# Performance work log

Hardware: AMD Instinct MI355X
Metric: run time of the kernel (lower is better)

The kernel has to match this reference:

```python
import jax, jax.numpy as jnp
import numpy as np

M, N, K, C, G = 16384, 131072, 16, 128, 8
EPS_BN = 1e-5


def _bn(x, g, b):
    # inference-mode BatchNorm1d (running_mean=0, running_var=1)
    return x * (g / jnp.sqrt(1.0 + EPS_BN)) + b


def setup_inputs() -> dict:
    key = jax.random.key(0)
    ks = jax.random.split(key, 16)
    f32 = jnp.float32
    s = 0.05
    return {
        "query_feat": jax.random.normal(ks[0], (M, C), f32),
        "context_feat": jax.random.normal(ks[1], (N, C), f32),
        "query_coord": jax.random.normal(ks[2], (M, 3), f32),
        "context_coord": jax.random.normal(ks[3], (N, 3), f32),
        "Wq": jax.random.normal(ks[4], (C, C), f32) * s,
        "bq": jnp.zeros((C,), f32),
        "gq": jnp.ones((C,), f32),
        "betaq": jnp.zeros((C,), f32),
        "Wk": jax.random.normal(ks[5], (C, C), f32) * s,
        "bk": jnp.zeros((C,), f32),
        "gk": jnp.ones((C,), f32),
        "betak": jnp.zeros((C,), f32),
        "Wv": jax.random.normal(ks[6], (C, C), f32) * s,
        "bv": jnp.zeros((C,), f32),
        "Wp1": jax.random.normal(ks[7], (3, C), f32) * s,
        "bp1": jnp.zeros((C,), f32),
        "gp1": jnp.ones((C,), f32),
        "betap1": jnp.zeros((C,), f32),
        "Wp2": jax.random.normal(ks[8], (C, C), f32) * s,
        "bp2": jnp.zeros((C,), f32),
        "Ww1": jax.random.normal(ks[9], (C, G), f32) * s,
        "bw1": jnp.zeros((G,), f32),
        "gw1": jnp.ones((G,), f32),
        "betaw1": jnp.zeros((G,), f32),
        "Ww2": jax.random.normal(ks[10], (G, G), f32) * s,
        "bw2": jnp.zeros((G,), f32),
        "knn_indexes": jax.random.randint(ks[11], (M, K), 0, N, dtype=jnp.int32),
    }


def reference(query_feat, context_feat, query_coord, context_coord,
              Wq, bq, gq, betaq, Wk, bk, gk, betak, Wv, bv,
              Wp1, bp1, gp1, betap1, Wp2, bp2,
              Ww1, bw1, gw1, betaw1, Ww2, bw2, knn_indexes):
    q = jax.nn.relu(_bn(query_feat @ Wq + bq, gq, betaq))              # (M, C)
    k = jax.nn.relu(_bn(context_feat @ Wk + bk, gk, betak))            # (N, C)
    v = context_feat @ Wv + bv                                         # (N, C)

    mask = knn_indexes >= 0                                            # (M, K); -1 = padded neighbor
    idx = jnp.where(mask, knn_indexes, 0)
    mf = mask[..., None].astype(q.dtype)                               # (M, K, 1)

    key_g = k[idx] * mf                                                # (M, K, C) gather (zero row for -1)
    val_g = v[idx] * mf                                                # (M, K, C)
    pos = (context_coord[idx] - query_coord[:, None, :]) * mf          # (M, K, 3) relative position

    # positional-encoding bias branch (pe_bias=True, pe_multiplier=False)
    peb = jax.nn.relu(_bn(pos @ Wp1 + bp1, gp1, betap1)) @ Wp2 + bp2   # (M, K, C)
    rel = key_g - q[:, None, :] + peb                                  # (M, K, C)
    val_g = val_g + peb

    # grouped vector attention weights
    w = jax.nn.relu(_bn(rel @ Ww1 + bw1, gw1, betaw1)) @ Ww2 + bw2     # (M, K, G)
    w = jax.nn.softmax(w, axis=1) * mf                                 # softmax over neighbors, mask padded

    m_, k_ = idx.shape
    c_ = q.shape[-1]
    g_ = w.shape[-1]
    out = jnp.einsum('mkgi,mkg->mgi', val_g.reshape(m_, k_, g_, c_ // g_), w)
    return out.reshape(m_, c_)
```

## Files before the change

### kernel.cpp

```cpp
#include <hip/hip_runtime.h>

#define C 128
#define G 8
#define KNN 16
#define QB 4
#define EPS 1e-5f

typedef unsigned short u16;
typedef __attribute__((ext_vector_type(8))) short short8;
typedef __attribute__((ext_vector_type(4))) float float4v;

union frag_u { short8 v; u16 u[8]; };

__device__ inline u16 f2bf(float f) {
    unsigned u = __builtin_bit_cast(unsigned, f);
    unsigned r = (u + 0x7fffu + ((u >> 16) & 1u)) >> 16;
    return (u16)r;
}
__device__ inline float bf2f(u16 h) {
    unsigned u = ((unsigned)h) << 16;
    return __builtin_bit_cast(float, u);
}

__global__ __launch_bounds__(256) void prep_w(
    const float* __restrict__ Wk, const float* __restrict__ Wv,
    const float* __restrict__ Wq, const float* __restrict__ Wp2,
    const float* __restrict__ Ww1, u16* __restrict__ dst)
{
    const int b = blockIdx.x, t = threadIdx.x;
    if (b < 4) {
        const float* W = b == 0 ? Wk : b == 1 ? Wv : b == 2 ? Wq : Wp2;
        u16* d = dst + b * 16384;
        for (int e = t; e < 16384; e += 256) {
            const int k = e >> 7, n = e & 127;
            const int cb = n >> 4, lan = n & 15;
            const int kk = k >> 5, quad = (k >> 3) & 3, j = k & 7;
            d[(((cb * 4 + kk) * 4 + quad) * 16 + lan) * 8 + j] = f2bf(W[e]);
        }
    } else {
        u16* d = dst + 4 * 16384;
        for (int e = t; e < 4096; e += 256) {
            const int j = e & 7, lan = (e >> 3) & 15;
            const int quad = (e >> 7) & 3, kk = e >> 9;
            const int k = kk * 32 + quad * 8 + j;
            d[e] = lan < 8 ? f2bf(Ww1[k * G + lan]) : (u16)0;
        }
    }
}

__global__ __launch_bounds__(256) void proj_kv(
    const float* __restrict__ X,
    const u16* __restrict__ PWk, const float* __restrict__ bk,
    const float* __restrict__ gk, const float* __restrict__ betak,
    const u16* __restrict__ PWv, const float* __restrict__ bv,
    u16* __restrict__ kout, u16* __restrict__ vout)
{
    __shared__ u16 Xs[64 * 136];
    __shared__ u16 Os[64 * 136];
    const int t = threadIdx.x;
    const int w = t >> 6, l = t & 63;
    const int quad = l >> 4, lan = l & 15;
    const long long row0 = (long long)blockIdx.x * 64;

    {
        const float4* Xv = (const float4*)(X + row0 * C);
#pragma unroll
        for (int i = 0; i < 8; i++) {
            const int e = t + 256 * i;
            const int r = e >> 5, c4 = e & 31;
            const float4 f = Xv[e];
            uint2 p;
            p.x = (unsigned)f2bf(f.x) | ((unsigned)f2bf(f.y) << 16);
            p.y = (unsigned)f2bf(f.z) | ((unsigned)f2bf(f.w) << 16);
            *(uint2*)(&Xs[r * 136 + c4 * 4]) = p;
        }
    }

    short8 Bf[2][2][4];
#pragma unroll
    for (int w2 = 0; w2 < 2; w2++) {
        const u16* P = w2 ? PWv : PWk;
#pragma unroll
        for (int ct = 0; ct < 2; ct++) {
            const int cb = w * 2 + ct;
#pragma unroll
            for (int kk = 0; kk < 4; kk++)
                Bf[w2][ct][kk] = *(const short8*)(P + (((cb * 4 + kk) * 4 + quad) * 16 + lan) * 8);
        }
    }
    __syncthreads();

    float4v acc[2][2][4];
#pragma unroll
    for (int w2 = 0; w2 < 2; w2++)
#pragma unroll
        for (int ct = 0; ct < 2; ct++)
#pragma unroll
            for (int rt = 0; rt < 4; rt++)
                acc[w2][ct][rt] = (float4v)0.f;

#pragma unroll
    for (int rt = 0; rt < 4; rt++) {
#pragma unroll
        for (int kk = 0; kk < 4; kk++) {
            const short8 A = *(const short8*)(&Xs[(rt * 16 + lan) * 136 + kk * 32 + quad * 8]);
#pragma unroll
            for (int w2 = 0; w2 < 2; w2++)
#pragma unroll
                for (int ct = 0; ct < 2; ct++)
                    acc[w2][ct][rt] = __builtin_amdgcn_mfma_f32_16x16x32_bf16(
                        A, Bf[w2][ct][kk], acc[w2][ct][rt], 0, 0, 0);
        }
    }

#pragma unroll
    for (int ct = 0; ct < 2; ct++) {
        const int cg = w * 32 + ct * 16 + lan;
        const float bb = bk[cg];
        const float sc = gk[cg] * rsqrtf(1.f + EPS);
        const float sh = betak[cg];
#pragma unroll
        for (int rt = 0; rt < 4; rt++)
#pragma unroll
            for (int reg = 0; reg < 4; reg++) {
                float y = (acc[0][ct][rt][reg] + bb) * sc + sh;
                y = y > 0.f ? y : 0.f;
                Os[(rt * 16 + quad * 4 + reg) * 136 + cg] = f2bf(y);
            }
    }
    __syncthreads();
#pragma unroll
    for (int i = 0; i < 4; i++) {
        const int e = t + 256 * i;
        const int r = e >> 4, cc = (e & 15) * 8;
        *(short8*)(kout + (row0 + r) * C + cc) = *(const short8*)(&Os[r * 136 + cc]);
    }
    __syncthreads();

#pragma unroll
    for (int ct = 0; ct < 2; ct++) {
        const int cg = w * 32 + ct * 16 + lan;
        const float bb = bv[cg];
#pragma unroll
        for (int rt = 0; rt < 4; rt++)
#pragma unroll
            for (int reg = 0; reg < 4; reg++)
                Os[(rt * 16 + quad * 4 + reg) * 136 + cg] = f2bf(acc[1][ct][rt][reg] + bb);
    }
    __syncthreads();
#pragma unroll
    for (int i = 0; i < 4; i++) {
        const int e = t + 256 * i;
        const int r = e >> 4, cc = (e & 15) * 8;
        *(short8*)(vout + (row0 + r) * C + cc) = *(const short8*)(&Os[r * 136 + cc]);
    }
}

__global__ __launch_bounds__(256) void attn4(
    const float* __restrict__ qfeat,
    const u16* __restrict__ kbuf, const u16* __restrict__ vbuf,
    const float* __restrict__ qcoord, const float* __restrict__ ccoord,
    const u16* __restrict__ PWq, const float* __restrict__ bq,
    const float* __restrict__ gq, const float* __restrict__ betaq,
    const float* __restrict__ Wp1, const float* __restrict__ bp1,
    const float* __restrict__ gp1, const float* __restrict__ betap1,
    const u16* __restrict__ PWp2, const float* __restrict__ bp2,
    const u16* __restrict__ PWw1, const float* __restrict__ bw1,
    const float* __restrict__ gw1, const float* __restrict__ betaw1,
    const float* __restrict__ Ww2, const float* __restrict__ bw2,
    const int* __restrict__ knn, float* __restrict__ out)
{
    __shared__ u16   fA[64 * 136];
    __shared__ u16   relB[64 * 136];
    __shared__ float qs[QB * C];
    __shared__ float pxs[64], pys[64], pzs[64], mfs[64];
    __shared__ float wl[QB * 16 * G];

    const int t = threadIdx.x;
    const int w = t >> 6, l = t & 63;
    const int quad = l >> 4, lan = l & 15;
    const int m0 = blockIdx.x * QB;

    const int rsub = t >> 4;
    const int c8 = (t & 15) * 8;
    float mfr[4];
    frag_u kg[4], vg[4];
#pragma unroll
    for (int p = 0; p < 4; p++) {
        const int ii = knn[m0 * KNN + p * 16 + rsub];
        mfr[p] = ii >= 0 ? 1.f : 0.f;
        const int i0 = ii >= 0 ? ii : 0;
        kg[p].v = *(const short8*)(kbuf + (size_t)i0 * C + c8);
        vg[p].v = *(const short8*)(vbuf + (size_t)i0 * C + c8);
    }

    {
        frag_u z;
        if (rsub < QB) {
            const float4 f0 = *(const float4*)(qfeat + (size_t)(m0 + rsub) * C + c8);
            const float4 f1 = *(const float4*)(qfeat + (size_t)(m0 + rsub) * C + c8 + 4);
            z.u[0] = f2bf(f0.x); z.u[1] = f2bf(f0.y);
            z.u[2] = f2bf(f0.z); z.u[3] = f2bf(f0.w);
            z.u[4] = f2bf(f1.x); z.u[5] = f2bf(f1.y);
            z.u[6] = f2bf(f1.z); z.u[7] = f2bf(f1.w);
        } else {
            z.v = (short8)0;
        }
        *(short8*)(&relB[rsub * 136 + c8]) = z.v;
    }
    if (t < 64) {
        const int q = t >> 4;
        const int ii = knn[m0 * KNN + t];
        const float mf = ii >= 0 ? 1.f : 0.f;
        const int i0 = ii >= 0 ? ii : 0;
        mfs[t] = mf;
        pxs[t] = (ccoord[i0 * 3 + 0] - qcoord[(m0 + q) * 3 + 0]) * mf;
        pys[t] = (ccoord[i0 * 3 + 1] - qcoord[(m0 + q) * 3 + 1]) * mf;
        pzs[t] = (ccoord[i0 * 3 + 2] - qcoord[(m0 + q) * 3 + 2]) * mf;
    }
    __syncthreads();

    {
        short8 Bq[2][4];
#pragma unroll
        for (int ct = 0; ct < 2; ct++) {
            const int cb = w * 2 + ct;
#pragma unroll
            for (int kk = 0; kk < 4; kk++)
                Bq[ct][kk] = *(const short8*)(PWq + (((cb * 4 + kk) * 4 + quad) * 16 + lan) * 8);
        }
        float4v aq[2];
        aq[0] = (float4v)0.f; aq[1] = (float4v)0.f;
#pragma unroll
        for (int kk = 0; kk < 4; kk++) {
            const short8 A = *(const short8*)(&relB[lan * 136 + kk * 32 + quad * 8]);
#pragma unroll
            for (int ct = 0; ct < 2; ct++)
                aq[ct] = __builtin_amdgcn_mfma_f32_16x16x32_bf16(A, Bq[ct][kk], aq[ct], 0, 0, 0);
        }
        if (quad == 0) {
#pragma unroll
            for (int ct = 0; ct < 2; ct++) {
                const int col = w * 32 + ct * 16 + lan;
                const float bb = bq[col];
                const float sc = gq[col] * rsqrtf(1.f + EPS);
                const float sh = betaq[col];
#pragma unroll
                for (int reg = 0; reg < 4; reg++) {
                    float y = (aq[ct][reg] + bb) * sc + sh;
                    qs[reg * C + col] = y > 0.f ? y : 0.f;
                }
            }
        }
    }

    {
        const int c = t & 127, hh = t >> 7;
        const float w0 = Wp1[c], w1_ = Wp1[C + c], w2_ = Wp1[2 * C + c];
        const float sc = gp1[c] * rsqrtf(1.f + EPS);
        const float bb = bp1[c], sh = betap1[c];
#pragma unroll
        for (int r2 = 0; r2 < 32; r2++) {
            const int r = hh * 32 + r2;
            float y = fmaf(pxs[r], w0, fmaf(pys[r], w1_, fmaf(pzs[r], w2_, bb)));
            y = y * sc + sh;
            y = y > 0.f ? y : 0.f;
            fA[r * 136 + c] = f2bf(y);
        }
    }
    __syncthreads();

    {
        short8 Bf[2][4];
#pragma unroll
        for (int ct = 0; ct < 2; ct++) {
            const int cb = w * 2 + ct;
#pragma unroll
            for (int kk = 0; kk < 4; kk++)
                Bf[ct][kk] = *(const short8*)(PWp2 + (((cb * 4 + kk) * 4 + quad) * 16 + lan) * 8);
        }
        float4v acc[2][4];
#pragma unroll
        for (int ct = 0; ct < 2; ct++)
#pragma unroll
            for (int q = 0; q < 4; q++) acc[ct][q] = (float4v)0.f;

#pragma unroll
        for (int q = 0; q < 4; q++) {
#pragma unroll
            for (int kk = 0; kk < 4; kk++) {
                const short8 A = *(const short8*)(&fA[(q * 16 + lan) * 136 + kk * 32 + quad * 8]);
#pragma unroll
                for (int ct = 0; ct < 2; ct++)
                    acc[ct][q] = __builtin_amdgcn_mfma_f32_16x16x32_bf16(
                        A, Bf[ct][kk], acc[ct][q], 0, 0, 0);
            }
        }
        const float bb0 = bp2[w * 32 + lan];
        const float bb1 = bp2[w * 32 + 16 + lan];
#pragma unroll
        for (int ct = 0; ct < 2; ct++)
#pragma unroll
            for (int q = 0; q < 4; q++)
#pragma unroll
                for (int reg = 0; reg < 4; reg++)
                    relB[(q * 16 + quad * 4 + reg) * 136 + w * 32 + ct * 16 + lan] =
                        f2bf(acc[ct][q][reg] + (ct ? bb1 : bb0));
    }
    __syncthreads();

    {
#pragma unroll
        for (int p = 0; p < 4; p++) {
            const int r = p * 16 + rsub;
            const float mf = mfr[p];
            frag_u peb, relv, valv;
            peb.v = *(const short8*)(&relB[r * 136 + c8]);
#pragma unroll
            for (int j = 0; j < 8; j++) {
                const float pe = bf2f(peb.u[j]);
                const float qv = qs[p * C + c8 + j];
                relv.u[j] = f2bf(fmaf(bf2f(kg[p].u[j]), mf, pe - qv));
                valv.u[j] = f2bf(fmaf(bf2f(vg[p].u[j]), mf, pe));
            }
            *(short8*)(&relB[r * 136 + c8]) = relv.v;
            *(short8*)(&fA[r * 136 + c8])  = valv.v;
        }
    }
    __syncthreads();

    {
        short8 Bw[4];
#pragma unroll
        for (int kk = 0; kk < 4; kk++)
            Bw[kk] = *(const short8*)(PWw1 + ((kk * 4 + quad) * 16 + lan) * 8);
        float4v acc = (float4v)0.f;
#pragma unroll
        for (int kk = 0; kk < 4; kk++) {
            const short8 A = *(const short8*)(&relB[(w * 16 + lan) * 136 + kk * 32 + quad * 8]);
            acc = __builtin_amdgcn_mfma_f32_16x16x32_bf16(A, Bw[kk], acc, 0, 0, 0);
        }
        if (lan < G) {
            const int g = lan;
            const float sc = gw1[g] * rsqrtf(1.f + EPS);
            const float bb = bw1[g], sh = betaw1[g];
#pragma unroll
            for (int reg = 0; reg < 4; reg++) {
                const int j = quad * 4 + reg;
                float y = (acc[reg] + bb) * sc + sh;
                wl[w * 128 + j * 8 + g] = y > 0.f ? y : 0.f;
            }
        }
    }
    __syncthreads();

    if (t < QB * G) {
        const int q = t >> 3, g2 = t & 7;
        float w2c[G];
#pragma unroll
        for (int g = 0; g < G; g++) w2c[g] = Ww2[g * G + g2];
        const float bb = bw2[g2];
        float lg[KNN], mx = -1e30f;
#pragma unroll
        for (int j = 0; j < KNN; j++) {
            float a = bb;
#pragma unroll
            for (int g = 0; g < G; g++) a = fmaf(wl[q * 128 + j * 8 + g], w2c[g], a);
            lg[j] = a;
            mx = fmaxf(mx, a);
        }
        float sum = 0.f;
#pragma unroll
        for (int j = 0; j < KNN; j++) { lg[j] = __expf(lg[j] - mx); sum += lg[j]; }
        const float inv = 1.f / sum;
#pragma unroll
        for (int j = 0; j < KNN; j++)
            wl[q * 128 + j * 8 + g2] = lg[j] * inv * mfs[q * 16 + j];
    }
    __syncthreads();

#pragma unroll
    for (int i = 0; i < 2; i++) {
        const int e = t + 256 * i;
        const int q = e >> 7, c = e & 127, g = c >> 4;
        float a = 0.f;
#pragma unroll
        for (int j = 0; j < KNN; j++)
            a = fmaf(bf2f(fA[(q * 16 + j) * 136 + c]), wl[q * 128 + j * 8 + g], a);
        out[(size_t)(m0 + q) * C + c] = a;
    }
}

extern "C" void kernel_launch(void* const* d_in, const int* in_sizes, int n_in,
                              void* d_out, int out_size, void* d_ws, size_t ws_size,
                              hipStream_t stream)
{
    const float* query_feat    = (const float*)d_in[0];
    const float* context_feat  = (const float*)d_in[1];
    const float* query_coord   = (const float*)d_in[2];
    const float* context_coord = (const float*)d_in[3];
    const float* Wq    = (const float*)d_in[4];
    const float* bq    = (const float*)d_in[5];
    const float* gq    = (const float*)d_in[6];
    const float* betaq = (const float*)d_in[7];
    const float* Wk    = (const float*)d_in[8];
    const float* bk    = (const float*)d_in[9];
    const float* gk    = (const float*)d_in[10];
    const float* betak = (const float*)d_in[11];
    const float* Wv    = (const float*)d_in[12];
    const float* bv    = (const float*)d_in[13];
    const float* Wp1   = (const float*)d_in[14];
    const float* bp1   = (const float*)d_in[15];
    const float* gp1   = (const float*)d_in[16];
    const float* betap1= (const float*)d_in[17];
    const float* Wp2   = (const float*)d_in[18];
    const float* bp2   = (const float*)d_in[19];
    const float* Ww1   = (const float*)d_in[20];
    const float* bw1   = (const float*)d_in[21];
    const float* gw1   = (const float*)d_in[22];
    const float* betaw1= (const float*)d_in[23];
    const float* Ww2   = (const float*)d_in[24];
    const float* bw2   = (const float*)d_in[25];
    const int*   knn   = (const int*)d_in[26];

    const int M = in_sizes[0] / C;
    const int N = in_sizes[1] / C;

    u16* kb = (u16*)d_ws;
    u16* vb = kb + (size_t)N * C;
    u16* pw = vb + (size_t)N * C;
    u16* pWk  = pw;
    u16* pWv  = pw + 16384;
    u16* pWq  = pw + 2 * 16384;
    u16* pWp2 = pw + 3 * 16384;
    u16* pWw1 = pw + 4 * 16384;

    prep_w<<<5, 256, 0, stream>>>(Wk, Wv, Wq, Wp2, Ww1, pw);
    proj_kv<<<N / 64, 256, 0, stream>>>(context_feat, pWk, bk, gk, betak,
                                        pWv, bv, kb, vb);
    attn4<<<M / QB, 256, 0, stream>>>(query_feat, kb, vb, query_coord, context_coord,
                                      pWq, bq, gq, betaq,
                                      Wp1, bp1, gp1, betap1, pWp2, bp2,
                                      pWw1, bw1, gw1, betaw1, Ww2, bw2,
                                      knn, (float*)d_out);
}
```

Baseline: 244.6 us.

## Move query projection into batched projection kernel and cut attention kernel LDS use

The query projection moves out of the attention kernel, where each block ran an MFMA on a mostly padded tile of 4 query rows, into the shared projection kernel. That kernel now also handles query row blocks and writes bf16 q to the workspace. The attention kernel drops the relB and qs buffers and the early k/v gathers, gathering k, v and q later from global memory, and reuses one LDS tile, which should lower LDS use and raise occupancy. The costs are extra global traffic for the q buffer, gathers that are no longer overlapped with early work, and a slightly different rounding of q to bf16. The weight prep kernel is also split across more blocks, and the projection kernel computes V and K one after the other to lower register pressure.

```diff
diff --git a/kernel.cpp b/kernel.cpp
--- a/kernel.cpp
+++ b/kernel.cpp
@@ -28,10 +28,11 @@
     const float* __restrict__ Ww1, u16* __restrict__ dst)
 {
     const int b = blockIdx.x, t = threadIdx.x;
-    if (b < 4) {
-        const float* W = b == 0 ? Wk : b == 1 ? Wv : b == 2 ? Wq : Wp2;
-        u16* d = dst + b * 16384;
-        for (int e = t; e < 16384; e += 256) {
+    if (b < 16) {
+        const int mi = b >> 2, qt = b & 3;
+        const float* W = mi == 0 ? Wk : mi == 1 ? Wv : mi == 2 ? Wq : Wp2;
+        u16* d = dst + mi * 16384;
+        for (int e = qt * 4096 + t; e < (qt + 1) * 4096; e += 256) {
             const int k = e >> 7, n = e & 127;
             const int cb = n >> 4, lan = n & 15;
             const int kk = k >> 5, quad = (k >> 3) & 3, j = k & 7;
@@ -48,19 +49,23 @@
     }
 }
 
-__global__ __launch_bounds__(256) void proj_kv(
-    const float* __restrict__ X,
+__global__ __launch_bounds__(256) void proj_all(
+    const float* __restrict__ Xc, const float* __restrict__ Xq,
     const u16* __restrict__ PWk, const float* __restrict__ bk,
     const float* __restrict__ gk, const float* __restrict__ betak,
     const u16* __restrict__ PWv, const float* __restrict__ bv,
-    u16* __restrict__ kout, u16* __restrict__ vout)
+    const u16* __restrict__ PWq, const float* __restrict__ bq,
+    const float* __restrict__ gq, const float* __restrict__ betaq,
+    u16* __restrict__ kout, u16* __restrict__ vout, u16* __restrict__ qout,
+    int nkv)
 {
     __shared__ u16 Xs[64 * 136];
-    __shared__ u16 Os[64 * 136];
     const int t = threadIdx.x;
     const int w = t >> 6, l = t & 63;
     const int quad = l >> 4, lan = l & 15;
-    const long long row0 = (long long)blockIdx.x * 64;
+    const bool isq = (int)blockIdx.x >= nkv;
+    const long long row0 = (long long)(isq ? blockIdx.x - nkv : blockIdx.x) * 64;
+    const float* X = isq ? Xq : Xc;
 
     {
         const float4* Xv = (const float4*)(X + row0 * C);
@@ -75,93 +80,168 @@
             *(uint2*)(&Xs[r * 136 + c4 * 4]) = p;
         }
     }
-
-    short8 Bf[2][2][4];
-#pragma unroll
-    for (int w2 = 0; w2 < 2; w2++) {
-        const u16* P = w2 ? PWv : PWk;
+    __syncthreads();
+
+    if (!isq) {
+        unsigned vp[2][4][2];
+        {
+            short8 Bf[2][4];
+#pragma unroll
+            for (int ct = 0; ct < 2; ct++) {
+                const int cb = w * 2 + ct;
+#pragma unroll
+                for (int kk = 0; kk < 4; kk++)
+                    Bf[ct][kk] = *(const short8*)(PWv + (((cb * 4 + kk) * 4 + quad) * 16 + lan) * 8);
+            }
+            float4v acc[2][4];
+#pragma unroll
+            for (int ct = 0; ct < 2; ct++)
+#pragma unroll
+                for (int rt = 0; rt < 4; rt++) acc[ct][rt] = (float4v)0.f;
+#pragma unroll
+            for (int rt = 0; rt < 4; rt++)
+#pragma unroll
+                for (int kk = 0; kk < 4; kk++) {
+                    const short8 A = *(const short8*)(&Xs[(rt * 16 + lan) * 136 + kk * 32 + quad * 8]);
+#pragma unroll
+                    for (int ct = 0; ct < 2; ct++)
+                        acc[ct][rt] = __builtin_amdgcn_mfma_f32_16x16x32_bf16(
+                            A, Bf[ct][kk], acc[ct][rt], 0, 0, 0);
+                }
+#pragma unroll
+            for (int ct = 0; ct < 2; ct++) {
+                const float bb = bv[w * 32 + ct * 16 + lan];
+#pragma unroll
+                for (int rt = 0; rt < 4; rt++)
+#pragma unroll
+                    for (int h = 0; h < 2; h++)
+                        vp[ct][rt][h] = (unsigned)f2bf(acc[ct][rt][2 * h] + bb)
+                                      | ((unsigned)f2bf(acc[ct][rt][2 * h + 1] + bb) << 16);
+            }
+        }
+        float4v acck[2][4];
+        {
+            short8 Bf[2][4];
+#pragma unroll
+            for (int ct = 0; ct < 2; ct++) {
+                const int cb = w * 2 + ct;
+#pragma unroll
+                for (int kk = 0; kk < 4; kk++)
+                    Bf[ct][kk] = *(const short8*)(PWk + (((cb * 4 + kk) * 4 + quad) * 16 + lan) * 8);
+            }
+#pragma unroll
+            for (int ct = 0; ct < 2; ct++)
+#pragma unroll
+                for (int rt = 0; rt < 4; rt++) acck[ct][rt] = (float4v)0.f;
+#pragma unroll
+            for (int rt = 0; rt < 4; rt++)
+#pragma unroll
+                for (int kk = 0; kk < 4; kk++) {
+                    const short8 A = *(const short8*)(&Xs[(rt * 16 + lan) * 136 + kk * 32 + quad * 8]);
+#pragma unroll
+                    for (int ct = 0; ct < 2; ct++)
+                        acck[ct][rt] = __builtin_amdgcn_mfma_f32_16x16x32_bf16(
+                            A, Bf[ct][kk], acck[ct][rt], 0, 0, 0);
+                }
+        }
+        __syncthreads();
+
+#pragma unroll
+        for (int ct = 0; ct < 2; ct++) {
+            const int cg = w * 32 + ct * 16 + lan;
+            const float bb = bk[cg];
+            const float sc = gk[cg] * rsqrtf(1.f + EPS);
+            const float sh = betak[cg];
+#pragma unroll
+            for (int rt = 0; rt < 4; rt++)
+#pragma unroll
+                for (int reg = 0; reg < 4; reg++) {
+                    float y = (acck[ct][rt][reg] + bb) * sc + sh;
+                    y = y > 0.f ? y : 0.f;
+                    Xs[(rt * 16 + quad * 4 + reg) * 136 + cg] = f2bf(y);
+                }
+        }
+        __syncthreads();
+#pragma unroll
+        for (int i = 0; i < 4; i++) {
+            const int e = t + 256 * i;
+            const int r = e >> 4, cc = (e & 15) * 8;
+            *(short8*)(kout + (row0 + r) * C + cc) = *(const short8*)(&Xs[r * 136 + cc]);
+        }
+        __syncthreads();
+
+#pragma unroll
+        for (int ct = 0; ct < 2; ct++) {
+            const int cg = w * 32 + ct * 16 + lan;
+#pragma unroll
+            for (int rt = 0; rt < 4; rt++)
+#pragma unroll
+                for (int h = 0; h < 2; h++) {
+                    Xs[(rt * 16 + quad * 4 + 2 * h) * 136 + cg]     = (u16)(vp[ct][rt][h] & 0xffffu);
+                    Xs[(rt * 16 + quad * 4 + 2 * h + 1) * 136 + cg] = (u16)(vp[ct][rt][h] >> 16);
+                }
+        }
+        __syncthreads();
+#pragma unroll
+        for (int i = 0; i < 4; i++) {
+            const int e = t + 256 * i;
+            const int r = e >> 4, cc = (e & 15) * 8;
+            *(short8*)(vout + (row0 + r) * C + cc) = *(const short8*)(&Xs[r * 136 + cc]);
+        }
+    } else {
+        short8 Bf[2][4];
 #pragma unroll
         for (int ct = 0; ct < 2; ct++) {
             const int cb = w * 2 + ct;
 #pragma unroll
             for (int kk = 0; kk < 4; kk++)
-                Bf[w2][ct][kk] = *(const short8*)(P + (((cb * 4 + kk) * 4 + quad) * 16 + lan) * 8);
-        }
-    }
-    __syncthreads();
-
-    float4v acc[2][2][4];
-#pragma unroll
-    for (int w2 = 0; w2 < 2; w2++)
+                Bf[ct][kk] = *(const short8*)(PWq + (((cb * 4 + kk) * 4 + quad) * 16 + lan) * 8);
+        }
+        float4v acc[2][4];
 #pragma unroll
         for (int ct = 0; ct < 2; ct++)
 #pragma unroll
+            for (int rt = 0; rt < 4; rt++) acc[ct][rt] = (float4v)0.f;
+#pragma unroll
+        for (int rt = 0; rt < 4; rt++)
+#pragma unroll
+            for (int kk = 0; kk < 4; kk++) {
+                const short8 A = *(const short8*)(&Xs[(rt * 16 + lan) * 136 + kk * 32 + quad * 8]);
+#pragma unroll
+                for (int ct = 0; ct < 2; ct++)
+                    acc[ct][rt] = __builtin_amdgcn_mfma_f32_16x16x32_bf16(
+                        A, Bf[ct][kk], acc[ct][rt], 0, 0, 0);
+            }
+        __syncthreads();
+#pragma unroll
+        for (int ct = 0; ct < 2; ct++) {
+            const int cg = w * 32 + ct * 16 + lan;
+            const float bb = bq[cg];
+            const float sc = gq[cg] * rsqrtf(1.f + EPS);
+            const float sh = betaq[cg];
+#pragma unroll
             for (int rt = 0; rt < 4; rt++)
-                acc[w2][ct][rt] = (float4v)0.f;
-
-#pragma unroll
-    for (int rt = 0; rt < 4; rt++) {
-#pragma unroll
-        for (int kk = 0; kk < 4; kk++) {
-            const short8 A = *(const short8*)(&Xs[(rt * 16 + lan) * 136 + kk * 32 + quad * 8]);
-#pragma unroll
-            for (int w2 = 0; w2 < 2; w2++)
-#pragma unroll
-                for (int ct = 0; ct < 2; ct++)
-                    acc[w2][ct][rt] = __builtin_amdgcn_mfma_f32_16x16x32_bf16(
-                        A, Bf[w2][ct][kk], acc[w2][ct][rt], 0, 0, 0);
-        }
-    }
-
-#pragma unroll
-    for (int ct = 0; ct < 2; ct++) {
-        const int cg = w * 32 + ct * 16 + lan;
-        const float bb = bk[cg];
-        const float sc = gk[cg] * rsqrtf(1.f + EPS);
-        const float sh = betak[cg];
-#pragma unroll
-        for (int rt = 0; rt < 4; rt++)
-#pragma unroll
-            for (int reg = 0; reg < 4; reg++) {
-                float y = (acc[0][ct][rt][reg] + bb) * sc + sh;
-                y = y > 0.f ? y : 0.f;
-                Os[(rt * 16 + quad * 4 + reg) * 136 + cg] = f2bf(y);
-            }
-    }
-    __syncthreads();
-#pragma unroll
-    for (int i = 0; i < 4; i++) {
-        const int e = t + 256 * i;
-        const int r = e >> 4, cc = (e & 15) * 8;
-        *(short8*)(kout + (row0 + r) * C + cc) = *(const short8*)(&Os[r * 136 + cc]);
-    }
-    __syncthreads();
-
-#pragma unroll
-    for (int ct = 0; ct < 2; ct++) {
-        const int cg = w * 32 + ct * 16 + lan;
-        const float bb = bv[cg];
-#pragma unroll
-        for (int rt = 0; rt < 4; rt++)
-#pragma unroll
-            for (int reg = 0; reg < 4; reg++)
-                Os[(rt * 16 + quad * 4 + reg) * 136 + cg] = f2bf(acc[1][ct][rt][reg] + bb);
-    }
-    __syncthreads();
-#pragma unroll
-    for (int i = 0; i < 4; i++) {
-        const int e = t + 256 * i;
-        const int r = e >> 4, cc = (e & 15) * 8;
-        *(short8*)(vout + (row0 + r) * C + cc) = *(const short8*)(&Os[r * 136 + cc]);
-    }
-}
-
-__global__ __launch_bounds__(256) void attn4(
-    const float* __restrict__ qfeat,
-    const u16* __restrict__ kbuf, const u16* __restrict__ vbuf,
+#pragma unroll
+                for (int reg = 0; reg < 4; reg++) {
+                    float y = (acc[ct][rt][reg] + bb) * sc + sh;
+                    y = y > 0.f ? y : 0.f;
+                    Xs[(rt * 16 + quad * 4 + reg) * 136 + cg] = f2bf(y);
+                }
+        }
+        __syncthreads();
+#pragma unroll
+        for (int i = 0; i < 4; i++) {
+            const int e = t + 256 * i;
+            const int r = e >> 4, cc = (e & 15) * 8;
+            *(short8*)(qout + (row0 + r) * C + cc) = *(const short8*)(&Xs[r * 136 + cc]);
+        }
+    }
+}
+
+__global__ __launch_bounds__(256) void attn5(
+    const u16* __restrict__ qbuf, const u16* __restrict__ kbuf,
+    const u16* __restrict__ vbuf,
     const float* __restrict__ qcoord, const float* __restrict__ ccoord,
-    const u16* __restrict__ PWq, const float* __restrict__ bq,
-    const float* __restrict__ gq, const float* __restrict__ betaq,
     const float* __restrict__ Wp1, const float* __restrict__ bp1,
     const float* __restrict__ gp1, const float* __restrict__ betap1,
     const u16* __restrict__ PWp2, const float* __restrict__ bp2,
@@ -171,88 +251,28 @@
     const int* __restrict__ knn, float* __restrict__ out)
 {
     __shared__ u16   fA[64 * 136];
-    __shared__ u16   relB[64 * 136];
-    __shared__ float qs[QB * C];
-    __shared__ float pxs[64], pys[64], pzs[64], mfs[64];
+    __shared__ float pxs[64], pys[64], pzs[64];
+    __shared__ int   idxs[64];
     __shared__ float wl[QB * 16 * G];
 
     const int t = threadIdx.x;
     const int w = t >> 6, l = t & 63;
     const int quad = l >> 4, lan = l & 15;
     const int m0 = blockIdx.x * QB;
-
     const int rsub = t >> 4;
     const int c8 = (t & 15) * 8;
-    float mfr[4];
-    frag_u kg[4], vg[4];
-#pragma unroll
-    for (int p = 0; p < 4; p++) {
-        const int ii = knn[m0 * KNN + p * 16 + rsub];
-        mfr[p] = ii >= 0 ? 1.f : 0.f;
-        const int i0 = ii >= 0 ? ii : 0;
-        kg[p].v = *(const short8*)(kbuf + (size_t)i0 * C + c8);
-        vg[p].v = *(const short8*)(vbuf + (size_t)i0 * C + c8);
-    }
-
-    {
-        frag_u z;
-        if (rsub < QB) {
-            const float4 f0 = *(const float4*)(qfeat + (size_t)(m0 + rsub) * C + c8);
-            const float4 f1 = *(const float4*)(qfeat + (size_t)(m0 + rsub) * C + c8 + 4);
-            z.u[0] = f2bf(f0.x); z.u[1] = f2bf(f0.y);
-            z.u[2] = f2bf(f0.z); z.u[3] = f2bf(f0.w);
-            z.u[4] = f2bf(f1.x); z.u[5] = f2bf(f1.y);
-            z.u[6] = f2bf(f1.z); z.u[7] = f2bf(f1.w);
-        } else {
-            z.v = (short8)0;
-        }
-        *(short8*)(&relB[rsub * 136 + c8]) = z.v;
-    }
+
     if (t < 64) {
         const int q = t >> 4;
-        const int ii = knn[m0 * KNN + t];
+        const int ii = knn[(m0 + q) * KNN + (t & 15)];
         const float mf = ii >= 0 ? 1.f : 0.f;
         const int i0 = ii >= 0 ? ii : 0;
-        mfs[t] = mf;
+        idxs[t] = ii;
         pxs[t] = (ccoord[i0 * 3 + 0] - qcoord[(m0 + q) * 3 + 0]) * mf;
         pys[t] = (ccoord[i0 * 3 + 1] - qcoord[(m0 + q) * 3 + 1]) * mf;
         pzs[t] = (ccoord[i0 * 3 + 2] - qcoord[(m0 + q) * 3 + 2]) * mf;
     }
     __syncthreads();
-
-    {
-        short8 Bq[2][4];
-#pragma unroll
-        for (int ct = 0; ct < 2; ct++) {
-            const int cb = w * 2 + ct;
-#pragma unroll
-            for (int kk = 0; kk < 4; kk++)
-                Bq[ct][kk] = *(const short8*)(PWq + (((cb * 4 + kk) * 4 + quad) * 16 + lan) * 8);
-        }
-        float4v aq[2];
-        aq[0] = (float4v)0.f; aq[1] = (float4v)0.f;
-#pragma unroll
-        for (int kk = 0; kk < 4; kk++) {
-            const short8 A = *(const short8*)(&relB[lan * 136 + kk * 32 + quad * 8]);
-#pragma unroll
-            for (int ct = 0; ct < 2; ct++)
-                aq[ct] = __builtin_amdgcn_mfma_f32_16x16x32_bf16(A, Bq[ct][kk], aq[ct], 0, 0, 0);
-        }
-        if (quad == 0) {
-#pragma unroll
-            for (int ct = 0; ct < 2; ct++) {
-                const int col = w * 32 + ct * 16 + lan;
-                const float bb = bq[col];
-                const float sc = gq[col] * rsqrtf(1.f + EPS);
-                const float sh = betaq[col];
-#pragma unroll
-                for (int reg = 0; reg < 4; reg++) {
-                    float y = (aq[ct][reg] + bb) * sc + sh;
-                    qs[reg * C + col] = y > 0.f ? y : 0.f;
-                }
-            }
-        }
-    }
 
     {
         const int c = t & 127, hh = t >> 7;
@@ -270,6 +290,7 @@
     }
     __syncthreads();
 
+    float4v acc[2][4];
     {
         short8 Bf[2][4];
 #pragma unroll
@@ -279,14 +300,12 @@
             for (int kk = 0; kk < 4; kk++)
                 Bf[ct][kk] = *(const short8*)(PWp2 + (((cb * 4 + kk) * 4 + quad) * 16 + lan) * 8);
         }
-        float4v acc[2][4];
 #pragma unroll
         for (int ct = 0; ct < 2; ct++)
 #pragma unroll
             for (int q = 0; q < 4; q++) acc[ct][q] = (float4v)0.f;
-
-#pragma unroll
-        for (int q = 0; q < 4; q++) {
+#pragma unroll
+        for (int q = 0; q < 4; q++)
 #pragma unroll
             for (int kk = 0; kk < 4; kk++) {
                 const short8 A = *(const short8*)(&fA[(q * 16 + lan) * 136 + kk * 32 + quad * 8]);
@@ -295,7 +314,10 @@
                     acc[ct][q] = __builtin_amdgcn_mfma_f32_16x16x32_bf16(
                         A, Bf[ct][kk], acc[ct][q], 0, 0, 0);
             }
-        }
+    }
+    __syncthreads();
+
+    {
         const float bb0 = bp2[w * 32 + lan];
         const float bb1 = bp2[w * 32 + 16 + lan];
 #pragma unroll
@@ -304,27 +326,32 @@
             for (int q = 0; q < 4; q++)
 #pragma unroll
                 for (int reg = 0; reg < 4; reg++)
-                    relB[(q * 16 + quad * 4 + reg) * 136 + w * 32 + ct * 16 + lan] =
+                    fA[(q * 16 + quad * 4 + reg) * 136 + w * 32 + ct * 16 + lan] =
                         f2bf(acc[ct][q][reg] + (ct ? bb1 : bb0));
     }
     __syncthreads();
 
+    short8 valr[4];
     {
 #pragma unroll
         for (int p = 0; p < 4; p++) {
             const int r = p * 16 + rsub;
-            const float mf = mfr[p];
-            frag_u peb, relv, valv;
-            peb.v = *(const short8*)(&relB[r * 136 + c8]);
+            const int ii = idxs[r];
+            const float mf = ii >= 0 ? 1.f : 0.f;
+            const size_t i0 = ii >= 0 ? ii : 0;
+            frag_u kgv, vgv, qgv, peb, relv, valv;
+            kgv.v = *(const short8*)(kbuf + i0 * C + c8);
+            vgv.v = *(const short8*)(vbuf + i0 * C + c8);
+            qgv.v = *(const short8*)(qbuf + (size_t)(m0 + p) * C + c8);
+            peb.v = *(const short8*)(&fA[r * 136 + c8]);
 #pragma unroll
             for (int j = 0; j < 8; j++) {
                 const float pe = bf2f(peb.u[j]);
-                const float qv = qs[p * C + c8 + j];
-                relv.u[j] = f2bf(fmaf(bf2f(kg[p].u[j]), mf, pe - qv));
-                valv.u[j] = f2bf(fmaf(bf2f(vg[p].u[j]), mf, pe));
-            }
-            *(short8*)(&relB[r * 136 + c8]) = relv.v;
-            *(short8*)(&fA[r * 136 + c8])  = valv.v;
+                relv.u[j] = f2bf(fmaf(bf2f(kgv.u[j]), mf, pe - bf2f(qgv.u[j])));
+                valv.u[j] = f2bf(fmaf(bf2f(vgv.u[j]), mf, pe));
+            }
+            *(short8*)(&fA[r * 136 + c8]) = relv.v;
+            valr[p] = valv.v;
         }
     }
     __syncthreads();
@@ -334,11 +361,11 @@
 #pragma unroll
         for (int kk = 0; kk < 4; kk++)
             Bw[kk] = *(const short8*)(PWw1 + ((kk * 4 + quad) * 16 + lan) * 8);
-        float4v acc = (float4v)0.f;
+        float4v a4 = (float4v)0.f;
 #pragma unroll
         for (int kk = 0; kk < 4; kk++) {
-            const short8 A = *(const short8*)(&relB[(w * 16 + lan) * 136 + kk * 32 + quad * 8]);
-            acc = __builtin_amdgcn_mfma_f32_16x16x32_bf16(A, Bw[kk], acc, 0, 0, 0);
+            const short8 A = *(const short8*)(&fA[(w * 16 + lan) * 136 + kk * 32 + quad * 8]);
+            a4 = __builtin_amdgcn_mfma_f32_16x16x32_bf16(A, Bw[kk], a4, 0, 0, 0);
         }
         if (lan < G) {
             const int g = lan;
@@ -347,12 +374,16 @@
 #pragma unroll
             for (int reg = 0; reg < 4; reg++) {
                 const int j = quad * 4 + reg;
-                float y = (acc[reg] + bb) * sc + sh;
+                float y = (a4[reg] + bb) * sc + sh;
                 wl[w * 128 + j * 8 + g] = y > 0.f ? y : 0.f;
             }
         }
     }
     __syncthreads();
+
+#pragma unroll
+    for (int p = 0; p < 4; p++)
+        *(short8*)(&fA[(p * 16 + rsub) * 136 + c8]) = valr[p];
 
     if (t < QB * G) {
         const int q = t >> 3, g2 = t & 7;
@@ -374,8 +405,10 @@
         for (int j = 0; j < KNN; j++) { lg[j] = __expf(lg[j] - mx); sum += lg[j]; }
         const float inv = 1.f / sum;
 #pragma unroll
-        for (int j = 0; j < KNN; j++)
-            wl[q * 128 + j * 8 + g2] = lg[j] * inv * mfs[q * 16 + j];
+        for (int j = 0; j < KNN; j++) {
+            const float mf = idxs[q * 16 + j] >= 0 ? 1.f : 0.f;
+            wl[q * 128 + j * 8 + g2] = lg[j] * inv * mf;
+        }
     }
     __syncthreads();
 
@@ -428,18 +461,21 @@
 
     u16* kb = (u16*)d_ws;
     u16* vb = kb + (size_t)N * C;
-    u16* pw = vb + (size_t)N * C;
+    u16* qb = vb + (size_t)N * C;
+    u16* pw = qb + (size_t)M * C;
     u16* pWk  = pw;
     u16* pWv  = pw + 16384;
     u16* pWq  = pw + 2 * 16384;
     u16* pWp2 = pw + 3 * 16384;
     u16* pWw1 = pw + 4 * 16384;
 
-    prep_w<<<5, 256, 0, stream>>>(Wk, Wv, Wq, Wp2, Ww1, pw);
-    proj_kv<<<N / 64, 256, 0, stream>>>(context_feat, pWk, bk, gk, betak,
-                                        pWv, bv, kb, vb);
-    attn4<<<M / QB, 256, 0, stream>>>(query_feat, kb, vb, query_coord, context_coord,
-                                      pWq, bq, gq, betaq,
+    prep_w<<<17, 256, 0, stream>>>(Wk, Wv, Wq, Wp2, Ww1, pw);
+    proj_all<<<N / 64 + M / 64, 256, 0, stream>>>(
+        context_feat, query_feat,
+        pWk, bk, gk, betak, pWv, bv,
+        pWq, bq, gq, betaq,
+        kb, vb, qb, N / 64);
+    attn5<<<M / QB, 256, 0, stream>>>(qb, kb, vb, query_coord, context_coord,
                                       Wp1, bp1, gp1, betap1, pWp2, bp2,
                                       pWw1, bw1, gw1, betaw1, Ww2, bw2,
                                       knn, (float*)d_out);
```

Result: faster. 225.5 us (-7.8%).
